# Optimization experiments

Measured on AMD Instinct MI355X. Metric: run time of the kernel, lower is better.

The kernel has to match this reference:

```python
import jax, jax.numpy as jnp
import numpy as np

N, D, H, IN, RD = 4096, 8, 64, 16, 32
B, S, K = 8, 16, 4

def setup_inputs() -> dict:
    key = jax.random.key(0)
    ks = jax.random.split(key, 24)
    rn = lambda k, shape, s=0.1: s * jax.random.normal(k, shape, dtype=jnp.float32)
    inp = {}
    inp["times"] = jnp.arange(S, dtype=jnp.float32) * 0.1
    inp["inputs"] = jax.random.normal(ks[0], (S, B, N, IN), dtype=jnp.float32)
    inp["h0"] = jax.random.normal(ks[1], (B, N, D), dtype=jnp.float32)
    inp["A"] = jax.random.uniform(ks[2], (N, N), dtype=jnp.float32) / N  # row-stochastic-ish graph operator
    inp["z"] = jax.random.normal(ks[3], (S - 1, K, B, N, D), dtype=jnp.float32)  # Brownian std-normal draws
    inp["drift_W1"] = rn(ks[4], (D + 1, H)); inp["drift_b1"] = jnp.zeros((H,), jnp.float32)
    inp["drift_W2"] = rn(ks[5], (H, D));     inp["drift_b2"] = jnp.zeros((D,), jnp.float32)
    inp["diff_W1"] = rn(ks[6], (D + 1, H));  inp["diff_b1"] = jnp.zeros((H,), jnp.float32)
    inp["diff_W2"] = rn(ks[7], (H, D));      inp["diff_b2"] = jnp.zeros((D,), jnp.float32)
    inp["pert_W1"] = rn(ks[8], (IN + D, H)); inp["pert_b1"] = jnp.zeros((H,), jnp.float32)
    inp["pert_W2"] = rn(ks[9], (H, D));      inp["pert_b2"] = jnp.zeros((D,), jnp.float32)
    inp["read_W1"] = rn(ks[10], (D, H));     inp["read_b1"] = jnp.zeros((H,), jnp.float32)
    inp["read_W2"] = rn(ks[11], (H, RD));    inp["read_b2"] = jnp.zeros((RD,), jnp.float32)
    return inp


def _forward(times, inputs, h0, A, z,
             drift_W1, drift_b1, drift_W2, drift_b2,
             diff_W1, diff_b1, diff_W2, diff_b2,
             pert_W1, pert_b1, pert_W2, pert_b2,
             read_W1, read_b1, read_W2, read_b2):
    Bb, Nn, Dd = h0.shape
    Kk = z.shape[1]

    def drift(t, h):  # h: [B,N,D]
        h_graph = jnp.einsum('ij,bjd->bid', A, h)  # graph message passing A @ h
        ht = jnp.concatenate([h_graph, jnp.broadcast_to(t, (Bb, Nn, 1))], axis=-1)
        return jnp.tanh(ht @ drift_W1 + drift_b1) @ drift_W2 + drift_b2

    def diffusion(t, h):  # diagonal noise magnitude
        ht = jnp.concatenate([h, jnp.broadcast_to(t, (Bb, Nn, 1))], axis=-1)
        d = jax.nn.sigmoid(ht @ diff_W1 + diff_b1) @ diff_W2 + diff_b2
        return 0.1 * jax.nn.sigmoid(d)

    def step(h, xs):
        x_i, t0, t1, z_i = xs  # z_i: [K,B,N,D]
        # instantaneous perturbation h(t+) = h(t-) + Perturb([x, h])
        comb = jnp.concatenate([x_i, h], axis=-1)
        delta = jax.nn.relu(comb @ pert_W1 + pert_b1) @ pert_W2 + pert_b2
        hp = h + delta
        dt = (t1 - t0) / Kk
        sqdt = jnp.sqrt(dt)
        def euler_sub(hk, kz):
            k_idx, zk = kz
            t = t0 + k_idx * dt
            hn = hk + drift(t, hk) * dt + diffusion(t, hk) * (sqdt * zk)
            return hn, None
        hp, _ = jax.lax.scan(euler_sub, hp, (jnp.arange(Kk, dtype=jnp.float32), z_i))
        return hp, hp

    _, traj = jax.lax.scan(step, h0, (inputs[:-1], times[:-1], times[1:], z))
    traj = jnp.concatenate([h0[None], traj], axis=0)  # [S,B,N,D]
    readouts = jax.nn.relu(traj @ read_W1 + read_b1) @ read_W2 + read_b2  # [S,B,N,RD]
    return traj, readouts


def reference(times, inputs, h0, A, z,
              drift_W1, drift_b1, drift_W2, drift_b2,
              diff_W1, diff_b1, diff_W2, diff_b2,
              pert_W1, pert_b1, pert_W2, pert_b2,
              read_W1, read_b1, read_W2, read_b2):
    return _forward(times, inputs, h0, A, z,
                    drift_W1, drift_b1, drift_W2, drift_b2,
                    diff_W1, diff_b1, diff_W2, diff_b2,
                    pert_W1, pert_b1, pert_W2, pert_b2,
                    read_W1, read_b1, read_W2, read_b2)
```

## Files before the change

kernel.cpp:

```cpp
#include <hip/hip_runtime.h>
#include <hip/hip_fp8.h>
#include <math.h>

typedef __attribute__((ext_vector_type(4))) float f32x4;

#define NN   4096
#define BB   8
#define DD   8
#define SS   16
#define KSUB 4
#define IND  16
#define NWG  256
#define TPB  1024
#define HSZ  (64 * 4096)
#define GSCALE 1.52587890625e-5f

__device__ __forceinline__ float fsig(float x) {
    return __builtin_amdgcn_rcpf(1.f + __expf(-x));
}
__device__ __forceinline__ float ftanh(float x) {
    x = fminf(fmaxf(x, -15.f), 15.f);
    float e = __expf(2.f * x);
    return (e - 1.f) * __builtin_amdgcn_rcpf(e + 1.f);
}
__device__ __forceinline__ unsigned char f2fp8(float x) {
    return __hip_cvt_float_to_fp8(x, __HIP_SATFINITE, __HIP_E4M3);
}

__global__ __launch_bounds__(256) void k_convA8(const float* __restrict__ A,
                                                unsigned char* __restrict__ A8,
                                                unsigned int* __restrict__ cnt) {
    if (blockIdx.x == 0)
        for (int idx = threadIdx.x; idx < 2048; idx += 256) cnt[idx] = 0u;
    size_t i = ((size_t)blockIdx.x * 256 + threadIdx.x) * 8;
    float4 v0 = *reinterpret_cast<const float4*>(A + i);
    float4 v1 = *reinterpret_cast<const float4*>(A + i + 4);
    unsigned char o[8];
    o[0] = f2fp8(v0.x * 65536.f); o[1] = f2fp8(v0.y * 65536.f);
    o[2] = f2fp8(v0.z * 65536.f); o[3] = f2fp8(v0.w * 65536.f);
    o[4] = f2fp8(v1.x * 65536.f); o[5] = f2fp8(v1.y * 65536.f);
    o[6] = f2fp8(v1.z * 65536.f); o[7] = f2fp8(v1.w * 65536.f);
    *reinterpret_cast<unsigned long long*>(&A8[i]) =
        *reinterpret_cast<const unsigned long long*>(o);
}

__device__ __forceinline__ void gbar3(unsigned int* cnt, int wg, int tid,
                                      unsigned int epoch) {
    unsigned int* ep = cnt + 1024;
    asm volatile("s_waitcnt vmcnt(0)" ::: "memory");
    __syncthreads();
    if (wg == 0) {
        if (tid == 0) {
            __hip_atomic_fetch_add(&cnt[0], 1u, __ATOMIC_RELAXED, __HIP_MEMORY_SCOPE_AGENT);
            for (;;) {
                unsigned int s = 0;
#pragma unroll
                for (int i = 0; i < 8; ++i)
                    s += __hip_atomic_load(&cnt[i * 32], __ATOMIC_RELAXED, __HIP_MEMORY_SCOPE_AGENT);
                if (s >= (unsigned int)NWG * epoch) break;
                __builtin_amdgcn_s_sleep(0);
            }
#pragma unroll
            for (int i = 0; i < 8; ++i)
                __hip_atomic_store(&ep[i * 32], epoch, __ATOMIC_RELAXED, __HIP_MEMORY_SCOPE_AGENT);
        }
    } else if (tid == 0) {
        __hip_atomic_fetch_add(&cnt[(wg & 7) * 32], 1u, __ATOMIC_RELAXED, __HIP_MEMORY_SCOPE_AGENT);
        while (__hip_atomic_load(&ep[(wg & 7) * 32], __ATOMIC_RELAXED, __HIP_MEMORY_SCOPE_AGENT) < epoch)
            __builtin_amdgcn_s_sleep(1);
    }
    __syncthreads();
    asm volatile("" ::: "memory");
}

struct PArgs {
    const unsigned char* A8;
    const float *times, *x_all, *z_all, *h0;
    const float *dW1, *db1, *dW2, *db2;
    const float *fW1, *fb1, *fW2, *fb2;
    const float *pW1, *pb1, *pW2, *pb2;
    float* traj;
    unsigned char* h8;
    unsigned int* cnt;
};

__global__ __launch_bounds__(TPB, 4) void k_persist(PArgs p) {
    __shared__ __align__(16) unsigned char ls_A8[16 * 4096];
    __shared__ float ls_part[8][16][68];
    __shared__ float ls_hold[16][68];
    __shared__ __align__(8) unsigned char ls_h8st[64][16];
    __shared__ float ls_dW1T[64][12]; __shared__ float ls_fW1T[64][12];
    __shared__ float ls_dW2[64][8];   __shared__ float ls_fW2[64][8];
    __shared__ float ls_pW1T[64][24]; __shared__ float ls_pW2[64][8];
    __shared__ float ls_db1[64];  __shared__ float ls_fb1[64];  __shared__ float ls_pb1[64];
    __shared__ float ls_db2[8];   __shared__ float ls_fb2[8];   __shared__ float ls_pb2[8];
    __shared__ float ls_times[SS];

    const int tid = threadIdx.x;
    const int wg  = blockIdx.x;
    const int i0  = (((wg & 7) << 5) | (wg >> 3)) << 4;
    const size_t myblk = (size_t)(i0 >> 4) << 10;

    for (int idx = tid; idx < 9*64; idx += TPB) {
        int d = idx >> 6, j = idx & 63;
        ls_dW1T[j][d] = p.dW1[idx]; ls_fW1T[j][d] = p.fW1[idx];
    }
    for (int idx = tid; idx < 64*8; idx += TPB) {
        ls_dW2[idx>>3][idx&7] = p.dW2[idx]; ls_fW2[idx>>3][idx&7] = p.fW2[idx];
        ls_pW2[idx>>3][idx&7] = p.pW2[idx];
    }
    for (int idx = tid; idx < 24*64; idx += TPB) ls_pW1T[idx&63][idx>>6] = p.pW1[idx];
    if (tid < 64) { ls_db1[tid] = p.db1[tid]; ls_fb1[tid] = p.fb1[tid]; ls_pb1[tid] = p.pb1[tid]; }
    else if (tid < 72) { ls_db2[tid-64] = p.db2[tid-64]; ls_fb2[tid-64] = p.fb2[tid-64]; ls_pb2[tid-64] = p.pb2[tid-64]; }
    else if (tid >= 128 && tid < 128 + SS) ls_times[tid-128] = p.times[tid-128];

    for (int it = 0; it < 8; ++it) {
        int gi = (it * TPB + tid) * 8;
        int node = gi >> 12, k = gi & 4095;
        unsigned long long v = *reinterpret_cast<const unsigned long long*>(
            p.A8 + (size_t)(i0 + node) * NN + k);
        *reinterpret_cast<unsigned long long*>(
            &ls_A8[(node << 12) + (k ^ ((node & 15) << 3))]) = v;
    }
    __syncthreads();

    const int q = tid & 7, row = tid >> 3;
    const int node = row & 15, b = row >> 4;

    {
        const float* hp = p.h0 + ((size_t)b * NN + i0 + node) * DD;
        float4 h0a = *reinterpret_cast<const float4*>(hp);
        float4 h0b = *reinterpret_cast<const float4*>(hp + 4);
        float hv[8] = {h0a.x,h0a.y,h0a.z,h0a.w,h0b.x,h0b.y,h0b.z,h0b.w};
        p.traj[((size_t)b * NN + i0 + node) * DD + q] = hv[q];

        float xin[24];
        const float* xp = p.x_all + ((size_t)b * NN + i0 + node) * IND;
        float4 x0 = *reinterpret_cast<const float4*>(xp);
        float4 x1 = *reinterpret_cast<const float4*>(xp + 4);
        float4 x2 = *reinterpret_cast<const float4*>(xp + 8);
        float4 x3 = *reinterpret_cast<const float4*>(xp + 12);
        xin[0]=x0.x; xin[1]=x0.y; xin[2]=x0.z; xin[3]=x0.w;
        xin[4]=x1.x; xin[5]=x1.y; xin[6]=x1.z; xin[7]=x1.w;
        xin[8]=x2.x; xin[9]=x2.y; xin[10]=x2.z; xin[11]=x2.w;
        xin[12]=x3.x; xin[13]=x3.y; xin[14]=x3.z; xin[15]=x3.w;
#pragma unroll
        for (int d = 0; d < 8; ++d) xin[16+d] = hv[d];

        float ap[8] = {0,0,0,0,0,0,0,0};
#pragma unroll
        for (int jj = 0; jj < 8; ++jj) {
            const int j = q + (jj << 3);
            float s1 = ls_pb1[j];
#pragma unroll
            for (int c4 = 0; c4 < 6; ++c4) {
                f32x4 wv = *reinterpret_cast<const f32x4*>(&ls_pW1T[j][c4*4]);
#pragma unroll
                for (int r = 0; r < 4; ++r) s1 += xin[c4*4+r] * wv[r];
            }
            s1 = fmaxf(s1, 0.f);
            f32x4 w2a = *reinterpret_cast<const f32x4*>(&ls_pW2[j][0]);
            f32x4 w2b = *reinterpret_cast<const f32x4*>(&ls_pW2[j][4]);
#pragma unroll
            for (int r = 0; r < 4; ++r) { ap[r] += s1*w2a[r]; ap[4+r] += s1*w2b[r]; }
        }
        float aps[8];
#pragma unroll
        for (int d = 0; d < 8; ++d) {
            float t = ap[d];
            t += __shfl_xor(t, 1); t += __shfl_xor(t, 2); t += __shfl_xor(t, 4);
            aps[d] = t;
        }
        float outp = hv[q] + aps[q] + ls_pb2[q];
        ls_hold[node][b*8 + q] = outp;
        ls_h8st[b*8 + q][node] = f2fp8(outp);
    }
    float4 zn0, zn1;
    {
        const size_t zb = ((size_t)b)*((size_t)NN*DD) + (size_t)(i0+node)*DD;
        zn0 = *reinterpret_cast<const float4*>(p.z_all + zb);
        zn1 = *reinterpret_cast<const float4*>(p.z_all + zb + 4);
    }
    __syncthreads();
    if (tid < 128) {
        int c = tid >> 1, j8 = (tid & 1) << 3;
        unsigned long long v = *reinterpret_cast<const unsigned long long*>(&ls_h8st[c][j8]);
        __hip_atomic_store(reinterpret_cast<unsigned long long*>(
            p.h8 + myblk + (c << 4) + j8), v,
            __ATOMIC_RELAXED, __HIP_MEMORY_SCOPE_AGENT);
    }
    gbar3(p.cnt, wg, tid, 1u);

    for (int g = 0; g < (SS-1)*KSUB; ++g) {
        const int s = g >> 2, k = g & 3;
        const unsigned char* hin  = p.h8 + (size_t)g * HSZ;
        unsigned char*       hout = p.h8 + (size_t)(g+1) * HSZ;

        const float t0 = ls_times[s], t1 = ls_times[s+1];
        const float dt = (t1 - t0) * 0.25f;
        const float tk = t0 + (float)k * dt;
        const float sqdt = sqrtf(dt);
        const bool dopert = (k == 3) && (s < SS - 2);

        {
            const int wave = tid >> 6, lane = tid & 63;
            const int k0 = wave << 8;
            const int lrow = lane & 15;
            const int ksub = (lane >> 4) << 3;
            const int abase = lrow << 12;
            const int axor  = (lrow & 15) << 3;
            f32x4 acc[4];
#pragma unroll
            for (int ct = 0; ct < 4; ++ct) acc[ct] = (f32x4){0.f,0.f,0.f,0.f};
#pragma unroll
            for (int kk = 0; kk < 8; ++kk) {
                const int koff = k0 + kk*32 + ksub;
                long bfr = *reinterpret_cast<const long*>(&ls_A8[abase + (koff ^ axor)]);
                const size_t hb = ((size_t)(koff >> 4) << 10) + (koff & 15);
#pragma unroll
                for (int ct = 0; ct < 4; ++ct) {
                    long av = *reinterpret_cast<const long*>(
                        hin + hb + ((ct*16 + lrow) << 4));
                    acc[ct] = __builtin_amdgcn_mfma_f32_16x16x32_fp8_fp8(
                        av, bfr, acc[ct], 0, 0, 0);
                }
            }
            const int rb = (lane >> 4) << 2;
            if (wave < 8) {
#pragma unroll
                for (int ct = 0; ct < 4; ++ct)
#pragma unroll
                    for (int r = 0; r < 4; ++r)
                        ls_part[wave][lrow][ct*16 + rb + r] = acc[ct][r];
            }
            __syncthreads();
            if (wave >= 8) {
#pragma unroll
                for (int ct = 0; ct < 4; ++ct)
#pragma unroll
                    for (int r = 0; r < 4; ++r)
                        ls_part[wave-8][lrow][ct*16 + rb + r] += acc[ct][r];
            }
            __syncthreads();
        }

        float ing[9], inh[9];
        {
            f32x4 g0 = (f32x4){0,0,0,0}, g1 = (f32x4){0,0,0,0};
#pragma unroll
            for (int w = 0; w < 8; ++w) {
                g0 += *reinterpret_cast<const f32x4*>(&ls_part[w][node][b*8]);
                g1 += *reinterpret_cast<const f32x4*>(&ls_part[w][node][b*8+4]);
            }
            f32x4 h0v = *reinterpret_cast<const f32x4*>(&ls_hold[node][b*8]);
            f32x4 h1v = *reinterpret_cast<const f32x4*>(&ls_hold[node][b*8+4]);
#pragma unroll
            for (int r = 0; r < 4; ++r) {
                ing[r] = g0[r]*GSCALE; ing[4+r] = g1[r]*GSCALE;
                inh[r] = h0v[r];       inh[4+r] = h1v[r];
            }
        }
        ing[8] = tk; inh[8] = tk;
        float adr[8] = {0,0,0,0,0,0,0,0}, adf[8] = {0,0,0,0,0,0,0,0};
#pragma unroll
        for (int jj = 0; jj < 8; ++jj) {
            const int j = q + (jj << 3);
            f32x4 w1a = *reinterpret_cast<const f32x4*>(&ls_dW1T[j][0]);
            f32x4 w1b = *reinterpret_cast<const f32x4*>(&ls_dW1T[j][4]);
            float w1t = ls_dW1T[j][8];
            f32x4 v1a = *reinterpret_cast<const f32x4*>(&ls_fW1T[j][0]);
            f32x4 v1b = *reinterpret_cast<const f32x4*>(&ls_fW1T[j][4]);
            float v1t = ls_fW1T[j][8];
            float s1 = ls_db1[j], s2 = ls_fb1[j];
#pragma unroll
            for (int r = 0; r < 4; ++r) {
                s1 += ing[r]*w1a[r] + ing[4+r]*w1b[r];
                s2 += inh[r]*v1a[r] + inh[4+r]*v1b[r];
            }
            s1 += ing[8]*w1t; s2 += inh[8]*v1t;
            float th = ftanh(s1), sg = fsig(s2);
            f32x4 w2a = *reinterpret_cast<const f32x4*>(&ls_dW2[j][0]);
            f32x4 w2b = *reinterpret_cast<const f32x4*>(&ls_dW2[j][4]);
            f32x4 v2a = *reinterpret_cast<const f32x4*>(&ls_fW2[j][0]);
            f32x4 v2b = *reinterpret_cast<const f32x4*>(&ls_fW2[j][4]);
#pragma unroll
            for (int r = 0; r < 4; ++r) {
                adr[r] += th*w2a[r]; adr[4+r] += th*w2b[r];
                adf[r] += sg*v2a[r]; adf[4+r] += sg*v2b[r];
            }
        }
#pragma unroll
        for (int d = 0; d < 8; ++d) {
            adr[d] += __shfl_xor(adr[d], 1); adr[d] += __shfl_xor(adr[d], 2); adr[d] += __shfl_xor(adr[d], 4);
            adf[d] += __shfl_xor(adf[d], 1); adf[d] += __shfl_xor(adf[d], 2); adf[d] += __shfl_xor(adf[d], 4);
        }
        float zz[8] = {zn0.x, zn0.y, zn0.z, zn0.w, zn1.x, zn1.y, zn1.z, zn1.w};
        float hnew[8];
#pragma unroll
        for (int d = 0; d < 8; ++d) {
            float dr  = adr[d] + ls_db2[d];
            float dif = 0.1f * fsig(adf[d] + ls_fb2[d]);
            hnew[d] = inh[d] + dr * dt + dif * (sqdt * zz[d]);
        }

        if (k == 3) {
            p.traj[((size_t)((s+1)*BB + b))*((size_t)NN*DD) + (size_t)(i0+node)*DD + q] = hnew[q];
        }
        float outv;
        if (dopert) {
            float xin[24];
            const float* xp = p.x_all + ((size_t)(s+1)*BB + b)*((size_t)NN*IND) + (size_t)(i0+node)*IND;
            float4 x0 = *reinterpret_cast<const float4*>(xp);
            float4 x1 = *reinterpret_cast<const float4*>(xp + 4);
            float4 x2 = *reinterpret_cast<const float4*>(xp + 8);
            float4 x3 = *reinterpret_cast<const float4*>(xp + 12);
            xin[0]=x0.x; xin[1]=x0.y; xin[2]=x0.z; xin[3]=x0.w;
            xin[4]=x1.x; xin[5]=x1.y; xin[6]=x1.z; xin[7]=x1.w;
            xin[8]=x2.x; xin[9]=x2.y; xin[10]=x2.z; xin[11]=x2.w;
            xin[12]=x3.x; xin[13]=x3.y; xin[14]=x3.z; xin[15]=x3.w;
#pragma unroll
            for (int d = 0; d < 8; ++d) xin[16+d] = hnew[d];
            float ap[8] = {0,0,0,0,0,0,0,0};
#pragma unroll
            for (int jj = 0; jj < 8; ++jj) {
                const int j = q + (jj << 3);
                float s1 = ls_pb1[j];
#pragma unroll
                for (int c4 = 0; c4 < 6; ++c4) {
                    f32x4 wv = *reinterpret_cast<const f32x4*>(&ls_pW1T[j][c4*4]);
#pragma unroll
                    for (int r = 0; r < 4; ++r) s1 += xin[c4*4+r] * wv[r];
                }
                s1 = fmaxf(s1, 0.f);
                f32x4 w2a = *reinterpret_cast<const f32x4*>(&ls_pW2[j][0]);
                f32x4 w2b = *reinterpret_cast<const f32x4*>(&ls_pW2[j][4]);
#pragma unroll
                for (int r = 0; r < 4; ++r) { ap[r] += s1*w2a[r]; ap[4+r] += s1*w2b[r]; }
            }
            float aps[8];
#pragma unroll
            for (int d = 0; d < 8; ++d) {
                float t = ap[d];
                t += __shfl_xor(t, 1); t += __shfl_xor(t, 2); t += __shfl_xor(t, 4);
                aps[d] = t;
            }
            outv = hnew[q] + aps[q] + ls_pb2[q];
        } else {
            outv = hnew[q];
        }
        ls_hold[node][b*8 + q] = outv;
        ls_h8st[b*8 + q][node] = f2fp8(outv);

        if (g + 1 < (SS-1)*KSUB) {
            const size_t zb = ((size_t)((g+1)*BB + b))*((size_t)NN*DD) + (size_t)(i0+node)*DD;
            zn0 = *reinterpret_cast<const float4*>(p.z_all + zb);
            zn1 = *reinterpret_cast<const float4*>(p.z_all + zb + 4);
        }
        if (g < (SS-1)*KSUB - 1) {
            __syncthreads();
            if (tid < 128) {
                int c = tid >> 1, j8 = (tid & 1) << 3;
                unsigned long long v = *reinterpret_cast<const unsigned long long*>(&ls_h8st[c][j8]);
                __hip_atomic_store(reinterpret_cast<unsigned long long*>(
                    hout + myblk + (c << 4) + j8), v,
                    __ATOMIC_RELAXED, __HIP_MEMORY_SCOPE_AGENT);
            }
            gbar3(p.cnt, wg, tid, (unsigned int)(g + 2));
        }
    }
}

__global__ __launch_bounds__(256) void k_readout(
    const float* __restrict__ traj,
    const float* __restrict__ rW1, const float* __restrict__ rb1,
    const float* __restrict__ rW2, const float* __restrict__ rb2,
    float* __restrict__ outr)
{
    __shared__ float ls_W1T[64][12];
    __shared__ float ls_W2[64][32];
    __shared__ float ls_b1[64];    __shared__ float ls_b2[32];
    const int tid = threadIdx.x;
    for (int idx = tid; idx < 8*64;  idx += 256) ls_W1T[idx&63][idx>>6] = rW1[idx];
    for (int idx = tid; idx < 64*32; idx += 256) ls_W2[idx>>5][idx&31] = rW2[idx];
    if (tid < 64) ls_b1[tid] = rb1[tid];
    else if (tid < 96) ls_b2[tid-64] = rb2[tid-64];
    __syncthreads();

    const int half = tid & 1, ob = half << 4;
    const size_t row = (size_t)blockIdx.x * 128 + (tid >> 1);
    const float4* pi = reinterpret_cast<const float4*>(traj + row*8);
    float4 a0 = pi[0], a1 = pi[1];
    float in[8] = {a0.x,a0.y,a0.z,a0.w,a1.x,a1.y,a1.z,a1.w};
    float out[16];
#pragma unroll
    for (int o4 = 0; o4 < 4; ++o4) {
        f32x4 bv = *reinterpret_cast<const f32x4*>(&ls_b2[ob + o4*4]);
#pragma unroll
        for (int r = 0; r < 4; ++r) out[o4*4+r] = bv[r];
    }
    for (int j = 0; j < 64; ++j) {
        f32x4 w1a = *reinterpret_cast<const f32x4*>(&ls_W1T[j][0]);
        f32x4 w1b = *reinterpret_cast<const f32x4*>(&ls_W1T[j][4]);
        float s1 = ls_b1[j];
#pragma unroll
        for (int r = 0; r < 4; ++r) s1 += in[r]*w1a[r] + in[4+r]*w1b[r];
        s1 = fmaxf(s1, 0.f);
#pragma unroll
        for (int o4 = 0; o4 < 4; ++o4) {
            f32x4 w2 = *reinterpret_cast<const f32x4*>(&ls_W2[j][ob + o4*4]);
#pragma unroll
            for (int r = 0; r < 4; ++r) out[o4*4+r] += s1 * w2[r];
        }
    }
    float* op = outr + row*32 + ob;
#pragma unroll
    for (int o4 = 0; o4 < 4; ++o4) {
        float4 v = {out[o4*4], out[o4*4+1], out[o4*4+2], out[o4*4+3]};
        *reinterpret_cast<float4*>(op + o4*4) = v;
    }
}

extern "C" void kernel_launch(void* const* d_in, const int* in_sizes, int n_in,
                              void* d_out, int out_size, void* d_ws, size_t ws_size,
                              hipStream_t stream) {
    (void)in_sizes; (void)n_in; (void)out_size; (void)ws_size;
    const float* times = (const float*)d_in[0];
    const float* x_all = (const float*)d_in[1];
    const float* h0    = (const float*)d_in[2];
    const float* Amat  = (const float*)d_in[3];
    const float* z_all = (const float*)d_in[4];
    const float* dW1 = (const float*)d_in[5],  *db1 = (const float*)d_in[6];
    const float* dW2 = (const float*)d_in[7],  *db2 = (const float*)d_in[8];
    const float* fW1 = (const float*)d_in[9],  *fb1 = (const float*)d_in[10];
    const float* fW2 = (const float*)d_in[11], *fb2 = (const float*)d_in[12];
    const float* pW1 = (const float*)d_in[13], *pb1 = (const float*)d_in[14];
    const float* pW2 = (const float*)d_in[15], *pb2 = (const float*)d_in[16];
    const float* rW1 = (const float*)d_in[17], *rb1 = (const float*)d_in[18];
    const float* rW2 = (const float*)d_in[19], *rb2 = (const float*)d_in[20];

    float* traj = (float*)d_out;
    float* outr = traj + (size_t)SS*BB*NN*DD;

    char* ws = (char*)d_ws;
    unsigned char* A8  = (unsigned char*)ws;
    unsigned char* h8  = (unsigned char*)(ws + (16u << 20));
    unsigned int*  cnt = (unsigned int*)(ws + (35u << 20));

    k_convA8<<<NN*NN/(256*8), 256, 0, stream>>>(Amat, A8, cnt);

    PArgs pa;
    pa.A8 = A8; pa.times = times; pa.x_all = x_all; pa.z_all = z_all; pa.h0 = h0;
    pa.dW1 = dW1; pa.db1 = db1; pa.dW2 = dW2; pa.db2 = db2;
    pa.fW1 = fW1; pa.fb1 = fb1; pa.fW2 = fW2; pa.fb2 = fb2;
    pa.pW1 = pW1; pa.pb1 = pb1; pa.pW2 = pW2; pa.pb2 = pb2;
    pa.traj = traj; pa.h8 = h8; pa.cnt = cnt;
    k_persist<<<NWG, TPB, 0, stream>>>(pa);

    k_readout<<<(SS*BB*NN)/128, 256, 0, stream>>>(traj, rW1, rb1, rW2, rb2, outr);
}
```

Measured before the change: 1.195 ms.

## Decentralize grid barrier, pack MLP weights as bf16, and prefetch global loads earlier

The grid barrier no longer routes through a master workgroup that sums the counters and broadcasts an epoch. Instead every workgroup polls the eight striped counters directly with a wave shuffle reduction, which removes one round trip of barrier latency per substep. MLP weights in LDS are now packed as bf16 pairs, halving LDS traffic for the weights at the cost of lower weight precision. The z and x loads are issued earlier to overlap with the graph matvec, and the traj store is deferred into the next iteration so it leaves the critical path before the barrier.

```diff
diff --git a/kernel.cpp b/kernel.cpp
--- a/kernel.cpp
+++ b/kernel.cpp
@@ -3,6 +3,7 @@
 #include <math.h>
 
 typedef __attribute__((ext_vector_type(4))) float f32x4;
+typedef __attribute__((ext_vector_type(4))) unsigned int u32x4;
 
 #define NN   4096
 #define BB   8
@@ -25,6 +26,11 @@
 }
 __device__ __forceinline__ unsigned char f2fp8(float x) {
     return __hip_cvt_float_to_fp8(x, __HIP_SATFINITE, __HIP_E4M3);
+}
+__device__ __forceinline__ float blo(unsigned int u) { return __uint_as_float(u << 16); }
+__device__ __forceinline__ float bhi(unsigned int u) { return __uint_as_float(u & 0xffff0000u); }
+__device__ __forceinline__ unsigned int bpack(float a, float b) {
+    return (__float_as_uint(a) >> 16) | (__float_as_uint(b) & 0xffff0000u);
 }
 
 __global__ __launch_bounds__(256) void k_convA8(const float* __restrict__ A,
@@ -44,30 +50,20 @@
         *reinterpret_cast<const unsigned long long*>(o);
 }
 
-__device__ __forceinline__ void gbar3(unsigned int* cnt, int wg, int tid,
+__device__ __forceinline__ void gbar4(unsigned int* cnt, int wg, int tid,
                                       unsigned int epoch) {
-    unsigned int* ep = cnt + 1024;
     asm volatile("s_waitcnt vmcnt(0)" ::: "memory");
     __syncthreads();
-    if (wg == 0) {
-        if (tid == 0) {
-            __hip_atomic_fetch_add(&cnt[0], 1u, __ATOMIC_RELAXED, __HIP_MEMORY_SCOPE_AGENT);
-            for (;;) {
-                unsigned int s = 0;
-#pragma unroll
-                for (int i = 0; i < 8; ++i)
-                    s += __hip_atomic_load(&cnt[i * 32], __ATOMIC_RELAXED, __HIP_MEMORY_SCOPE_AGENT);
-                if (s >= (unsigned int)NWG * epoch) break;
-                __builtin_amdgcn_s_sleep(0);
-            }
-#pragma unroll
-            for (int i = 0; i < 8; ++i)
-                __hip_atomic_store(&ep[i * 32], epoch, __ATOMIC_RELAXED, __HIP_MEMORY_SCOPE_AGENT);
-        }
-    } else if (tid == 0) {
+    if (tid == 0)
         __hip_atomic_fetch_add(&cnt[(wg & 7) * 32], 1u, __ATOMIC_RELAXED, __HIP_MEMORY_SCOPE_AGENT);
-        while (__hip_atomic_load(&ep[(wg & 7) * 32], __ATOMIC_RELAXED, __HIP_MEMORY_SCOPE_AGENT) < epoch)
+    if (tid < 8) {
+        const unsigned int target = (unsigned int)NWG * epoch;
+        for (;;) {
+            unsigned int v = __hip_atomic_load(&cnt[tid * 32], __ATOMIC_RELAXED, __HIP_MEMORY_SCOPE_AGENT);
+            v += __shfl_xor(v, 1); v += __shfl_xor(v, 2); v += __shfl_xor(v, 4);
+            if (v >= target) break;
             __builtin_amdgcn_s_sleep(1);
+        }
     }
     __syncthreads();
     asm volatile("" ::: "memory");
@@ -89,9 +85,12 @@
     __shared__ float ls_part[8][16][68];
     __shared__ float ls_hold[16][68];
     __shared__ __align__(8) unsigned char ls_h8st[64][16];
-    __shared__ float ls_dW1T[64][12]; __shared__ float ls_fW1T[64][12];
-    __shared__ float ls_dW2[64][8];   __shared__ float ls_fW2[64][8];
-    __shared__ float ls_pW1T[64][24]; __shared__ float ls_pW2[64][8];
+    __shared__ __align__(16) unsigned int ls_dW1P[64][8];
+    __shared__ __align__(16) unsigned int ls_fW1P[64][8];
+    __shared__ __align__(16) unsigned int ls_dW2P[64][4];
+    __shared__ __align__(16) unsigned int ls_fW2P[64][4];
+    __shared__ __align__(16) unsigned int ls_pW1P[64][12];
+    __shared__ __align__(16) unsigned int ls_pW2P[64][4];
     __shared__ float ls_db1[64];  __shared__ float ls_fb1[64];  __shared__ float ls_pb1[64];
     __shared__ float ls_db2[8];   __shared__ float ls_fb2[8];   __shared__ float ls_pb2[8];
     __shared__ float ls_times[SS];
@@ -101,15 +100,24 @@
     const int i0  = (((wg & 7) << 5) | (wg >> 3)) << 4;
     const size_t myblk = (size_t)(i0 >> 4) << 10;
 
-    for (int idx = tid; idx < 9*64; idx += TPB) {
-        int d = idx >> 6, j = idx & 63;
-        ls_dW1T[j][d] = p.dW1[idx]; ls_fW1T[j][d] = p.fW1[idx];
-    }
-    for (int idx = tid; idx < 64*8; idx += TPB) {
-        ls_dW2[idx>>3][idx&7] = p.dW2[idx]; ls_fW2[idx>>3][idx&7] = p.fW2[idx];
-        ls_pW2[idx>>3][idx&7] = p.pW2[idx];
-    }
-    for (int idx = tid; idx < 24*64; idx += TPB) ls_pW1T[idx&63][idx>>6] = p.pW1[idx];
+    for (int idx = tid; idx < 64 * 5; idx += TPB) {
+        int j = idx & 63, r = idx >> 6;
+        float a0 = p.dW1[(2*r)*64 + j], b0 = p.fW1[(2*r)*64 + j];
+        float a1 = (r < 4) ? p.dW1[(2*r+1)*64 + j] : 0.f;
+        float b1 = (r < 4) ? p.fW1[(2*r+1)*64 + j] : 0.f;
+        ls_dW1P[j][r] = bpack(a0, a1);
+        ls_fW1P[j][r] = bpack(b0, b1);
+    }
+    for (int idx = tid; idx < 64 * 4; idx += TPB) {
+        int j = idx & 63, r = idx >> 6;
+        ls_dW2P[j][r] = bpack(p.dW2[j*8 + 2*r], p.dW2[j*8 + 2*r + 1]);
+        ls_fW2P[j][r] = bpack(p.fW2[j*8 + 2*r], p.fW2[j*8 + 2*r + 1]);
+        ls_pW2P[j][r] = bpack(p.pW2[j*8 + 2*r], p.pW2[j*8 + 2*r + 1]);
+    }
+    for (int idx = tid; idx < 64 * 12; idx += TPB) {
+        int j = idx & 63, r = idx >> 6;
+        ls_pW1P[j][r] = bpack(p.pW1[(2*r)*64 + j], p.pW1[(2*r+1)*64 + j]);
+    }
     if (tid < 64) { ls_db1[tid] = p.db1[tid]; ls_fb1[tid] = p.fb1[tid]; ls_pb1[tid] = p.pb1[tid]; }
     else if (tid < 72) { ls_db2[tid-64] = p.db2[tid-64]; ls_fb2[tid-64] = p.fb2[tid-64]; ls_pb2[tid-64] = p.pb2[tid-64]; }
     else if (tid >= 128 && tid < 128 + SS) ls_times[tid-128] = p.times[tid-128];
@@ -151,18 +159,23 @@
 #pragma unroll
         for (int jj = 0; jj < 8; ++jj) {
             const int j = q + (jj << 3);
+            u32x4 P0 = *reinterpret_cast<const u32x4*>(&ls_pW1P[j][0]);
+            u32x4 P1 = *reinterpret_cast<const u32x4*>(&ls_pW1P[j][4]);
+            u32x4 P2 = *reinterpret_cast<const u32x4*>(&ls_pW1P[j][8]);
             float s1 = ls_pb1[j];
 #pragma unroll
-            for (int c4 = 0; c4 < 6; ++c4) {
-                f32x4 wv = *reinterpret_cast<const f32x4*>(&ls_pW1T[j][c4*4]);
-#pragma unroll
-                for (int r = 0; r < 4; ++r) s1 += xin[c4*4+r] * wv[r];
+            for (int r = 0; r < 4; ++r) {
+                s1 += xin[2*r]*blo(P0[r])    + xin[2*r+1]*bhi(P0[r]);
+                s1 += xin[8+2*r]*blo(P1[r])  + xin[9+2*r]*bhi(P1[r]);
+                s1 += xin[16+2*r]*blo(P2[r]) + xin[17+2*r]*bhi(P2[r]);
             }
             s1 = fmaxf(s1, 0.f);
-            f32x4 w2a = *reinterpret_cast<const f32x4*>(&ls_pW2[j][0]);
-            f32x4 w2b = *reinterpret_cast<const f32x4*>(&ls_pW2[j][4]);
-#pragma unroll
-            for (int r = 0; r < 4; ++r) { ap[r] += s1*w2a[r]; ap[4+r] += s1*w2b[r]; }
+            u32x4 Q = *reinterpret_cast<const u32x4*>(&ls_pW2P[j][0]);
+#pragma unroll
+            for (int r = 0; r < 4; ++r) {
+                ap[2*r]   += s1 * blo(Q[r]);
+                ap[2*r+1] += s1 * bhi(Q[r]);
+            }
         }
         float aps[8];
 #pragma unroll
@@ -189,18 +202,31 @@
             p.h8 + myblk + (c << 4) + j8), v,
             __ATOMIC_RELAXED, __HIP_MEMORY_SCOPE_AGENT);
     }
-    gbar3(p.cnt, wg, tid, 1u);
+    gbar4(p.cnt, wg, tid, 1u);
+
+    float trajv = 0.f; size_t taddr = 0; bool thave = false;
 
     for (int g = 0; g < (SS-1)*KSUB; ++g) {
         const int s = g >> 2, k = g & 3;
         const unsigned char* hin  = p.h8 + (size_t)g * HSZ;
         unsigned char*       hout = p.h8 + (size_t)(g+1) * HSZ;
+
+        if (thave) { p.traj[taddr] = trajv; thave = false; }
 
         const float t0 = ls_times[s], t1 = ls_times[s+1];
         const float dt = (t1 - t0) * 0.25f;
         const float tk = t0 + (float)k * dt;
         const float sqdt = sqrtf(dt);
         const bool dopert = (k == 3) && (s < SS - 2);
+
+        float4 xv0, xv1, xv2, xv3;
+        if (dopert) {
+            const float* xp = p.x_all + ((size_t)(s+1)*BB + b)*((size_t)NN*IND) + (size_t)(i0+node)*IND;
+            xv0 = *reinterpret_cast<const float4*>(xp);
+            xv1 = *reinterpret_cast<const float4*>(xp + 4);
+            xv2 = *reinterpret_cast<const float4*>(xp + 8);
+            xv3 = *reinterpret_cast<const float4*>(xp + 12);
+        }
 
         {
             const int wave = tid >> 6, lane = tid & 63;
@@ -244,6 +270,13 @@
             __syncthreads();
         }
 
+        float4 zp0, zp1;
+        if (g + 1 < (SS-1)*KSUB) {
+            const size_t zb = ((size_t)((g+1)*BB + b))*((size_t)NN*DD) + (size_t)(i0+node)*DD;
+            zp0 = *reinterpret_cast<const float4*>(p.z_all + zb);
+            zp1 = *reinterpret_cast<const float4*>(p.z_all + zb + 4);
+        }
+
         float ing[9], inh[9];
         {
             f32x4 g0 = (f32x4){0,0,0,0}, g1 = (f32x4){0,0,0,0};
@@ -265,28 +298,23 @@
 #pragma unroll
         for (int jj = 0; jj < 8; ++jj) {
             const int j = q + (jj << 3);
-            f32x4 w1a = *reinterpret_cast<const f32x4*>(&ls_dW1T[j][0]);
-            f32x4 w1b = *reinterpret_cast<const f32x4*>(&ls_dW1T[j][4]);
-            float w1t = ls_dW1T[j][8];
-            f32x4 v1a = *reinterpret_cast<const f32x4*>(&ls_fW1T[j][0]);
-            f32x4 v1b = *reinterpret_cast<const f32x4*>(&ls_fW1T[j][4]);
-            float v1t = ls_fW1T[j][8];
+            u32x4 A1 = *reinterpret_cast<const u32x4*>(&ls_dW1P[j][0]);
+            u32x4 B1 = *reinterpret_cast<const u32x4*>(&ls_fW1P[j][0]);
             float s1 = ls_db1[j], s2 = ls_fb1[j];
 #pragma unroll
             for (int r = 0; r < 4; ++r) {
-                s1 += ing[r]*w1a[r] + ing[4+r]*w1b[r];
-                s2 += inh[r]*v1a[r] + inh[4+r]*v1b[r];
-            }
-            s1 += ing[8]*w1t; s2 += inh[8]*v1t;
+                s1 += ing[2*r]*blo(A1[r]) + ing[2*r+1]*bhi(A1[r]);
+                s2 += inh[2*r]*blo(B1[r]) + inh[2*r+1]*bhi(B1[r]);
+            }
+            s1 += ing[8]*blo(ls_dW1P[j][4]);
+            s2 += inh[8]*blo(ls_fW1P[j][4]);
             float th = ftanh(s1), sg = fsig(s2);
-            f32x4 w2a = *reinterpret_cast<const f32x4*>(&ls_dW2[j][0]);
-            f32x4 w2b = *reinterpret_cast<const f32x4*>(&ls_dW2[j][4]);
-            f32x4 v2a = *reinterpret_cast<const f32x4*>(&ls_fW2[j][0]);
-            f32x4 v2b = *reinterpret_cast<const f32x4*>(&ls_fW2[j][4]);
+            u32x4 C2 = *reinterpret_cast<const u32x4*>(&ls_dW2P[j][0]);
+            u32x4 D2 = *reinterpret_cast<const u32x4*>(&ls_fW2P[j][0]);
 #pragma unroll
             for (int r = 0; r < 4; ++r) {
-                adr[r] += th*w2a[r]; adr[4+r] += th*w2b[r];
-                adf[r] += sg*v2a[r]; adf[4+r] += sg*v2b[r];
+                adr[2*r]   += th*blo(C2[r]); adr[2*r+1] += th*bhi(C2[r]);
+                adf[2*r]   += sg*blo(D2[r]); adf[2*r+1] += sg*bhi(D2[r]);
             }
         }
 #pragma unroll
@@ -304,38 +332,39 @@
         }
 
         if (k == 3) {
-            p.traj[((size_t)((s+1)*BB + b))*((size_t)NN*DD) + (size_t)(i0+node)*DD + q] = hnew[q];
+            taddr = ((size_t)((s+1)*BB + b))*((size_t)NN*DD) + (size_t)(i0+node)*DD + q;
+            trajv = hnew[q]; thave = true;
         }
         float outv;
         if (dopert) {
             float xin[24];
-            const float* xp = p.x_all + ((size_t)(s+1)*BB + b)*((size_t)NN*IND) + (size_t)(i0+node)*IND;
-            float4 x0 = *reinterpret_cast<const float4*>(xp);
-            float4 x1 = *reinterpret_cast<const float4*>(xp + 4);
-            float4 x2 = *reinterpret_cast<const float4*>(xp + 8);
-            float4 x3 = *reinterpret_cast<const float4*>(xp + 12);
-            xin[0]=x0.x; xin[1]=x0.y; xin[2]=x0.z; xin[3]=x0.w;
-            xin[4]=x1.x; xin[5]=x1.y; xin[6]=x1.z; xin[7]=x1.w;
-            xin[8]=x2.x; xin[9]=x2.y; xin[10]=x2.z; xin[11]=x2.w;
-            xin[12]=x3.x; xin[13]=x3.y; xin[14]=x3.z; xin[15]=x3.w;
+            xin[0]=xv0.x; xin[1]=xv0.y; xin[2]=xv0.z; xin[3]=xv0.w;
+            xin[4]=xv1.x; xin[5]=xv1.y; xin[6]=xv1.z; xin[7]=xv1.w;
+            xin[8]=xv2.x; xin[9]=xv2.y; xin[10]=xv2.z; xin[11]=xv2.w;
+            xin[12]=xv3.x; xin[13]=xv3.y; xin[14]=xv3.z; xin[15]=xv3.w;
 #pragma unroll
             for (int d = 0; d < 8; ++d) xin[16+d] = hnew[d];
             float ap[8] = {0,0,0,0,0,0,0,0};
 #pragma unroll
             for (int jj = 0; jj < 8; ++jj) {
                 const int j = q + (jj << 3);
+                u32x4 P0 = *reinterpret_cast<const u32x4*>(&ls_pW1P[j][0]);
+                u32x4 P1 = *reinterpret_cast<const u32x4*>(&ls_pW1P[j][4]);
+                u32x4 P2 = *reinterpret_cast<const u32x4*>(&ls_pW1P[j][8]);
                 float s1 = ls_pb1[j];
 #pragma unroll
-                for (int c4 = 0; c4 < 6; ++c4) {
-                    f32x4 wv = *reinterpret_cast<const f32x4*>(&ls_pW1T[j][c4*4]);
-#pragma unroll
-                    for (int r = 0; r < 4; ++r) s1 += xin[c4*4+r] * wv[r];
+                for (int r = 0; r < 4; ++r) {
+                    s1 += xin[2*r]*blo(P0[r])    + xin[2*r+1]*bhi(P0[r]);
+                    s1 += xin[8+2*r]*blo(P1[r])  + xin[9+2*r]*bhi(P1[r]);
+                    s1 += xin[16+2*r]*blo(P2[r]) + xin[17+2*r]*bhi(P2[r]);
                 }
                 s1 = fmaxf(s1, 0.f);
-                f32x4 w2a = *reinterpret_cast<const f32x4*>(&ls_pW2[j][0]);
-                f32x4 w2b = *reinterpret_cast<const f32x4*>(&ls_pW2[j][4]);
-#pragma unroll
-                for (int r = 0; r < 4; ++r) { ap[r] += s1*w2a[r]; ap[4+r] += s1*w2b[r]; }
+                u32x4 Q = *reinterpret_cast<const u32x4*>(&ls_pW2P[j][0]);
+#pragma unroll
+                for (int r = 0; r < 4; ++r) {
+                    ap[2*r]   += s1 * blo(Q[r]);
+                    ap[2*r+1] += s1 * bhi(Q[r]);
+                }
             }
             float aps[8];
 #pragma unroll
@@ -350,12 +379,8 @@
         }
         ls_hold[node][b*8 + q] = outv;
         ls_h8st[b*8 + q][node] = f2fp8(outv);
-
-        if (g + 1 < (SS-1)*KSUB) {
-            const size_t zb = ((size_t)((g+1)*BB + b))*((size_t)NN*DD) + (size_t)(i0+node)*DD;
-            zn0 = *reinterpret_cast<const float4*>(p.z_all + zb);
-            zn1 = *reinterpret_cast<const float4*>(p.z_all + zb + 4);
-        }
+        zn0 = zp0; zn1 = zp1;
+
         if (g < (SS-1)*KSUB - 1) {
             __syncthreads();
             if (tid < 128) {
@@ -365,9 +390,10 @@
                     hout + myblk + (c << 4) + j8), v,
                     __ATOMIC_RELAXED, __HIP_MEMORY_SCOPE_AGENT);
             }
-            gbar3(p.cnt, wg, tid, (unsigned int)(g + 2));
-        }
-    }
+            gbar4(p.cnt, wg, tid, (unsigned int)(g + 2));
+        }
+    }
+    if (thave) { p.traj[taddr] = trajv; }
 }
 
 __global__ __launch_bounds__(256) void k_readout(
```

Result: slower. 2.276 ms (+90.4%).
